# Kernel optimization log

Measured on AMD Instinct MI355X. Metric: run time of the kernel, lower is better.

## Reference

```python
import jax, jax.numpy as jnp
import numpy as np

H, W = 8, 8
N = 1 + H * W          # 65 tokens (cls + patches)
DIM = 128
HEADS = 8
DH = 32
INNER = HEADS * DH     # 256
B = 64
EPS = 1e-5


def setup_inputs() -> dict:
    key = jax.random.key(0)
    ks = jax.random.split(key, 7)
    x = jax.random.normal(ks[0], (B, N, DIM), dtype=jnp.float32)
    gamma = jnp.ones((DIM,), jnp.float32)
    beta = jnp.zeros((DIM,), jnp.float32)
    # kaiming_uniform-ish init scale for linear weights
    s_qk = float(np.sqrt(1.0 / DIM))
    Wqk = jax.random.uniform(ks[1], (DIM, 2 * INNER), jnp.float32, -s_qk, s_qk)
    # per-(query, key)-position value weights: [n, n, dim, inner]
    Wv = jax.random.uniform(ks[2], (N, N, DIM, INNER), jnp.float32, -s_qk, s_qk)
    s_o = float(np.sqrt(1.0 / INNER))
    Wout = jax.random.uniform(ks[3], (INNER, DIM), jnp.float32, -s_o, s_o)
    bout = jax.random.uniform(ks[4], (DIM,), jnp.float32, -s_o, s_o)
    return {"x": x, "gamma": gamma, "beta": beta, "Wqk": Wqk, "Wv": Wv,
            "Wout": Wout, "bout": bout}


def reference(x, gamma, beta, Wqk, Wv, Wout, bout):
    b, n, d = x.shape
    # LayerNorm
    mu = jnp.mean(x, axis=-1, keepdims=True)
    var = jnp.mean(jnp.square(x - mu), axis=-1, keepdims=True)
    xn = (x - mu) / jnp.sqrt(var + EPS) * gamma + beta
    # q, k projections
    qk = xn @ Wqk                               # [b, n, 2*inner]
    q, k = jnp.split(qk, 2, axis=-1)
    q = q.reshape(b, n, HEADS, DH).transpose(0, 2, 1, 3)  # [b, h, n, dh]
    k = k.reshape(b, n, HEADS, DH).transpose(0, 2, 1, 3)
    scale = DH ** -0.5
    dots = jnp.einsum('bhnd,bhmd->bhnm', q, k) * scale
    attn = jax.nn.softmax(dots, axis=-1)        # [b, h, n, m]
    # per-(n,m) value: v[b,n,m] = xn[b,n] @ Wv[n,m]  -> [b, n, m, inner]
    v = jnp.einsum('bnd,nmde->bnme', xn, Wv)
    v = v.reshape(b, n, n, HEADS, DH)           # [b, n, m, h, dh]
    # weighted sum over keys m
    out = jnp.einsum('bhnm,bnmhd->bnhd', attn, v).reshape(b, n, INNER)
    return out @ Wout + bout
```

## Files before the change

kernel.cpp:

```cpp
#include <hip/hip_runtime.h>

#define EPS 1e-5f

typedef __attribute__((ext_vector_type(8))) short short8;
typedef __attribute__((ext_vector_type(4))) float float4v;

__device__ __forceinline__ unsigned short f2bf(float x) {
  unsigned int u = __builtin_bit_cast(unsigned int, x);
  u += 0x7fffu + ((u >> 16) & 1u);
  return (unsigned short)(u >> 16);
}
__device__ __forceinline__ float bf2f(unsigned short h) {
  unsigned int u = ((unsigned int)h) << 16;
  return __builtin_bit_cast(float, u);
}

__global__ __launch_bounds__(256) void ln_kernel(
    const float* __restrict__ x, const float* __restrict__ gamma,
    const float* __restrict__ beta, float* __restrict__ xn) {
  const int row = blockIdx.x * 4 + (threadIdx.x >> 6);
  const int lane = threadIdx.x & 63;
  const float2 v = ((const float2*)(x + (size_t)row * 128))[lane];
  float s = v.x + v.y;
#pragma unroll
  for (int off = 1; off < 64; off <<= 1) s += __shfl_xor(s, off);
  const float mu = s * (1.f / 128.f);
  const float dx = v.x - mu, dy = v.y - mu;
  float qv = dx * dx + dy * dy;
#pragma unroll
  for (int off = 1; off < 64; off <<= 1) qv += __shfl_xor(qv, off);
  const float rstd = 1.f / sqrtf(qv * (1.f / 128.f) + EPS);
  const float2 g = ((const float2*)gamma)[lane];
  const float2 be = ((const float2*)beta)[lane];
  float2 o;
  o.x = dx * rstd * g.x + be.x;
  o.y = dy * rstd * g.y + be.y;
  ((float2*)(xn + (size_t)row * 128))[lane] = o;
}

__global__ __launch_bounds__(256) void qk_kernel(
    const float* __restrict__ xn, const float* __restrict__ Wqk,
    float* __restrict__ qk) {
  __shared__ float xsx[32][130];
  __shared__ float wsx[128][68];
  const int t = threadIdx.x;
  const int r0 = blockIdx.x * 32, c0 = blockIdx.y * 64;
  for (int i = t; i < 32 * 32; i += 256) {
    int r = i >> 5, c = (i & 31) << 2;
    float4 v = *(const float4*)(xn + (size_t)(r0 + r) * 128 + c);
    float* dst = &xsx[r][c];
    dst[0] = v.x; dst[1] = v.y; dst[2] = v.z; dst[3] = v.w;
  }
  for (int i = t; i < 128 * 16; i += 256) {
    int k = i >> 4, c = (i & 15) << 2;
    *(float4*)&wsx[k][c] = *(const float4*)(Wqk + (size_t)k * 512 + c0 + c);
  }
  __syncthreads();
  const int rr = (t >> 4) * 2, cc = (t & 15) * 4;
  float acc[2][4] = {{0.f, 0.f, 0.f, 0.f}, {0.f, 0.f, 0.f, 0.f}};
  for (int k = 0; k < 128; k++) {
    float4 wv4 = *(const float4*)&wsx[k][cc];
    float x0 = xsx[rr][k], x1 = xsx[rr + 1][k];
    acc[0][0] += x0 * wv4.x; acc[0][1] += x0 * wv4.y;
    acc[0][2] += x0 * wv4.z; acc[0][3] += x0 * wv4.w;
    acc[1][0] += x1 * wv4.x; acc[1][1] += x1 * wv4.y;
    acc[1][2] += x1 * wv4.z; acc[1][3] += x1 * wv4.w;
  }
#pragma unroll
  for (int r = 0; r < 2; r++) {
    float4 o;
    o.x = acc[r][0]; o.y = acc[r][1]; o.z = acc[r][2]; o.w = acc[r][3];
    *(float4*)(qk + (size_t)(r0 + rr + r) * 512 + c0 + cc) = o;
  }
}

__global__ __launch_bounds__(256) void softmax_kernel(
    const float* __restrict__ qk, float* __restrict__ attn) {
  const int b = blockIdx.x >> 3, h = blockIdx.x & 7;
  __shared__ float qs[65][33];
  __shared__ float ks[65][33];
  __shared__ float dotsS[65][66];
  __shared__ float rsum[65];
  const int t = threadIdx.x;
  for (int i = t; i < 65 * 32; i += 256) {
    int n = i >> 5, d = i & 31;
    size_t base = ((size_t)b * 65 + n) * 512 + h * 32 + d;
    qs[n][d] = qk[base];
    ks[n][d] = qk[base + 256];
  }
  __syncthreads();
  const float scale = 0.17677669529663687f;
  for (int i = t; i < 65 * 65; i += 256) {
    int n = i / 65, mm = i - n * 65;
    float s = 0.f;
#pragma unroll
    for (int d = 0; d < 32; d++) s += qs[n][d] * ks[mm][d];
    dotsS[n][mm] = s * scale;
  }
  __syncthreads();
  if (t < 65) {
    float mx = -1e30f;
    for (int mm = 0; mm < 65; mm++) mx = fmaxf(mx, dotsS[t][mm]);
    float sum = 0.f;
    for (int mm = 0; mm < 65; mm++) {
      float e = __expf(dotsS[t][mm] - mx);
      dotsS[t][mm] = e;
      sum += e;
    }
    rsum[t] = 1.f / sum;
  }
  __syncthreads();
  const size_t obase = ((size_t)b * 8 + h) * 65 * 65;
  for (int i = t; i < 65 * 65; i += 256) {
    int n = i / 65;
    attn[obase + i] = dotsS[n][i - n * 65] * rsum[n];
  }
}

__global__ __launch_bounds__(256, 3) void attnv_kernel(
    const float* __restrict__ xn, const float* __restrict__ attn,
    const float* __restrict__ Wv, float* __restrict__ inner) {
  __shared__ __align__(16) char sbuf[33280];
  __shared__ float attnL[4225];
  float* xs = (float*)sbuf;
  unsigned short* wvb = (unsigned short*)sbuf;

  const int nq = blockIdx.x >> 3, h = blockIdx.x & 7;
  const int t = threadIdx.x, lane = t & 63, w = t >> 6;
  const int boff = w * 16;
  const int er = lane & 15, q = lane >> 4;

  const int e = t & 31;
  const int d0 = (t >> 5) * 16;
  const int kc0 = d0 >> 3;
  const float* wbase = Wv + (size_t)nq * 65 * 32768 + (size_t)h * 32 + e;

  float stg[16];
  {
    const float* p = wbase + (size_t)d0 * 256;
#pragma unroll
    for (int i = 0; i < 16; i++) stg[i] = p[(size_t)i * 256];
  }

  for (int i = t; i < 64 * 65; i += 256) {
    int b = i / 65, m = i - b * 65;
    attnL[m * 65 + b] = attn[(((size_t)b * 8 + h) * 65 + nq) * 65 + m];
  }
  for (int i = t; i < 64 * 32; i += 256) {
    int b = i >> 5, c = (i & 31) << 2;
    float4 v = *(const float4*)(xn + ((size_t)b * 65 + nq) * 128 + c);
    float* dst = xs + b * 130 + c;
    dst[0] = v.x; dst[1] = v.y; dst[2] = v.z; dst[3] = v.w;
  }
  __syncthreads();

  short8 ah[4], al[4];
  {
    const int arow = boff + er;
#pragma unroll
    for (int s = 0; s < 4; s++) {
#pragma unroll
      for (int j = 0; j < 8; j++) {
        float xv = xs[arow * 130 + s * 32 + q * 8 + j];
        unsigned short hi = f2bf(xv);
        ah[s][j] = (short)hi;
        al[s][j] = (short)f2bf(xv - bf2f(hi));
      }
    }
  }
  __syncthreads();

  {
    short8 w0, w1;
#pragma unroll
    for (int j = 0; j < 8; j++) {
      w0[j] = (short)f2bf(stg[j]);
      w1[j] = (short)f2bf(stg[8 + j]);
    }
    *(short8*)&wvb[e * 128 + ((kc0 ^ (e & 15)) << 3)] = w0;
    *(short8*)&wvb[e * 128 + (((kc0 + 1) ^ (e & 15)) << 3)] = w1;
  }
  __syncthreads();

  float4v acc0 = {0.f, 0.f, 0.f, 0.f}, acc1 = {0.f, 0.f, 0.f, 0.f};

  for (int m = 0; m < 65; m++) {
    const int cur = m & 1;
    if (m < 64) {
      const float* p = wbase + (size_t)(m + 1) * 32768 + (size_t)d0 * 256;
#pragma unroll
      for (int i = 0; i < 16; i++) stg[i] = p[(size_t)i * 256];
    }
    const unsigned short* wb = wvb + cur * 4096;
    float4v P0 = {0.f, 0.f, 0.f, 0.f}, P1 = {0.f, 0.f, 0.f, 0.f};
#pragma unroll
    for (int s = 0; s < 4; s++) {
      const int kc = 4 * s + q;
      short8 b0 = *(const short8*)&wb[er * 128 + ((kc ^ er) << 3)];
      short8 b1 = *(const short8*)&wb[(er + 16) * 128 + ((kc ^ er) << 3)];
      P0 = __builtin_amdgcn_mfma_f32_16x16x32_bf16(ah[s], b0, P0, 0, 0, 0);
      P1 = __builtin_amdgcn_mfma_f32_16x16x32_bf16(ah[s], b1, P1, 0, 0, 0);
      P0 = __builtin_amdgcn_mfma_f32_16x16x32_bf16(al[s], b0, P0, 0, 0, 0);
      P1 = __builtin_amdgcn_mfma_f32_16x16x32_bf16(al[s], b1, P1, 0, 0, 0);
    }
    {
      const float* ap = attnL + m * 65 + boff + q * 4;
#pragma unroll
      for (int r = 0; r < 4; r++) {
        float av = ap[r];
        acc0[r] += av * P0[r];
        acc1[r] += av * P1[r];
      }
    }
    if (m < 64) {
      short8 w0, w1;
#pragma unroll
      for (int j = 0; j < 8; j++) {
        w0[j] = (short)f2bf(stg[j]);
        w1[j] = (short)f2bf(stg[8 + j]);
      }
      unsigned short* wbw = wvb + (1 - cur) * 4096;
      *(short8*)&wbw[e * 128 + ((kc0 ^ (e & 15)) << 3)] = w0;
      *(short8*)&wbw[e * 128 + (((kc0 + 1) ^ (e & 15)) << 3)] = w1;
    }
    __syncthreads();
  }

#pragma unroll
  for (int r = 0; r < 4; r++) {
    int b = boff + q * 4 + r;
    size_t o = ((size_t)b * 65 + nq) * 256 + h * 32;
    inner[o + er] = acc0[r];
    inner[o + 16 + er] = acc1[r];
  }
}

__global__ __launch_bounds__(256) void outproj_kernel(
    const float* __restrict__ inner, const float* __restrict__ Wout,
    const float* __restrict__ bout, float* __restrict__ out) {
  __shared__ float isx[16][258];
  __shared__ float wsx[64][132];
  const int t = threadIdx.x;
  const int r0 = blockIdx.x * 16;
  for (int i = t; i < 16 * 64; i += 256) {
    int r = i >> 6, c = (i & 63) << 2;
    float4 v = *(const float4*)(inner + (size_t)(r0 + r) * 256 + c);
    float* dst = &isx[r][c];
    dst[0] = v.x; dst[1] = v.y; dst[2] = v.z; dst[3] = v.w;
  }
  const int rr = (t >> 5) * 2, cc = (t & 31) * 4;
  float acc[2][4] = {{0.f, 0.f, 0.f, 0.f}, {0.f, 0.f, 0.f, 0.f}};
  for (int kc = 0; kc < 4; kc++) {
    __syncthreads();
    for (int i = t; i < 64 * 32; i += 256) {
      int k = i >> 5, c = (i & 31) << 2;
      *(float4*)&wsx[k][c] = *(const float4*)(Wout + (size_t)(kc * 64 + k) * 128 + c);
    }
    __syncthreads();
#pragma unroll 8
    for (int k = 0; k < 64; k++) {
      float4 wv4 = *(const float4*)&wsx[k][cc];
      float x0 = isx[rr][kc * 64 + k];
      float x1 = isx[rr + 1][kc * 64 + k];
      acc[0][0] += x0 * wv4.x; acc[0][1] += x0 * wv4.y;
      acc[0][2] += x0 * wv4.z; acc[0][3] += x0 * wv4.w;
      acc[1][0] += x1 * wv4.x; acc[1][1] += x1 * wv4.y;
      acc[1][2] += x1 * wv4.z; acc[1][3] += x1 * wv4.w;
    }
  }
  float4 bb = *(const float4*)(bout + cc);
#pragma unroll
  for (int r = 0; r < 2; r++) {
    float4 o;
    o.x = acc[r][0] + bb.x; o.y = acc[r][1] + bb.y;
    o.z = acc[r][2] + bb.z; o.w = acc[r][3] + bb.w;
    *(float4*)(out + (size_t)(r0 + rr + r) * 128 + cc) = o;
  }
}

extern "C" void kernel_launch(void* const* d_in, const int* in_sizes, int n_in,
                              void* d_out, int out_size, void* d_ws, size_t ws_size,
                              hipStream_t stream) {
  const float* x     = (const float*)d_in[0];
  const float* gamma = (const float*)d_in[1];
  const float* beta  = (const float*)d_in[2];
  const float* Wqk   = (const float*)d_in[3];
  const float* Wv    = (const float*)d_in[4];
  const float* Wout  = (const float*)d_in[5];
  const float* bout  = (const float*)d_in[6];
  float* out = (float*)d_out;
  float* ws  = (float*)d_ws;

  float* xn    = ws;
  float* qk    = ws + 532480;
  float* attn  = ws + 2662400;
  float* inner = ws + 4825600;

  ln_kernel<<<1040, 256, 0, stream>>>(x, gamma, beta, xn);
  qk_kernel<<<dim3(130, 8), 256, 0, stream>>>(xn, Wqk, qk);
  softmax_kernel<<<512, 256, 0, stream>>>(qk, attn);
  attnv_kernel<<<520, 256, 0, stream>>>(xn, attn, Wv, inner);
  outproj_kernel<<<260, 256, 0, stream>>>(inner, Wout, bout, out);
}
```

Before: 807.7 us.

## Split attnv key loop across two blocks and transpose attn layout

The attention-value kernel now splits the 65 key positions into two halves handled by separate blocks, doubling the grid to 1040 blocks. Each half writes a partial inner buffer, and the output projection sums the two. Softmax writes attention transposed so attnv can load its slice contiguously, and xn is read straight from global memory instead of being staged in LDS. Shared memory drops and the occupancy hint rises to 4. The aim is more parallelism for streaming the large Wv tensor, at the cost of an extra partial buffer and scattered, strided writes in softmax.

```diff
diff --git a/kernel.cpp b/kernel.cpp
--- a/kernel.cpp
+++ b/kernel.cpp
@@ -75,7 +75,7 @@
 }
 
 __global__ __launch_bounds__(256) void softmax_kernel(
-    const float* __restrict__ qk, float* __restrict__ attn) {
+    const float* __restrict__ qk, float* __restrict__ attnT) {
   const int b = blockIdx.x >> 3, h = blockIdx.x & 7;
   __shared__ float qs[65][33];
   __shared__ float ks[65][33];
@@ -110,22 +110,24 @@
     rsum[t] = 1.f / sum;
   }
   __syncthreads();
-  const size_t obase = ((size_t)b * 8 + h) * 65 * 65;
   for (int i = t; i < 65 * 65; i += 256) {
-    int n = i / 65;
-    attn[obase + i] = dotsS[n][i - n * 65] * rsum[n];
-  }
-}
-
-__global__ __launch_bounds__(256, 3) void attnv_kernel(
-    const float* __restrict__ xn, const float* __restrict__ attn,
-    const float* __restrict__ Wv, float* __restrict__ inner) {
-  __shared__ __align__(16) char sbuf[33280];
-  __shared__ float attnL[4225];
-  float* xs = (float*)sbuf;
-  unsigned short* wvb = (unsigned short*)sbuf;
-
-  const int nq = blockIdx.x >> 3, h = blockIdx.x & 7;
+    int n = i / 65, mm = i - n * 65;
+    attnT[(((size_t)h * 65 + n) * 65 + mm) * 64 + b] = dotsS[n][mm] * rsum[n];
+  }
+}
+
+__global__ __launch_bounds__(256, 4) void attnv_kernel(
+    const float* __restrict__ xn, const float* __restrict__ attnT,
+    const float* __restrict__ Wv, float* __restrict__ innerp) {
+  __shared__ __align__(16) unsigned short wvb[2][4096];
+  __shared__ float attnL[33 * 64];
+
+  const int nq = blockIdx.x >> 4;
+  const int h = (blockIdx.x >> 1) & 7;
+  const int half = blockIdx.x & 1;
+  const int m0 = half * 33;
+  const int mlen = half ? 32 : 33;
+
   const int t = threadIdx.x, lane = t & 63, w = t >> 6;
   const int boff = w * 16;
   const int er = lane & 15, q = lane >> 4;
@@ -133,7 +135,7 @@
   const int e = t & 31;
   const int d0 = (t >> 5) * 16;
   const int kc0 = d0 >> 3;
-  const float* wbase = Wv + (size_t)nq * 65 * 32768 + (size_t)h * 32 + e;
+  const float* wbase = Wv + ((size_t)nq * 65 + m0) * 32768 + (size_t)h * 32 + e;
 
   float stg[16];
   {
@@ -142,33 +144,27 @@
     for (int i = 0; i < 16; i++) stg[i] = p[(size_t)i * 256];
   }
 
-  for (int i = t; i < 64 * 65; i += 256) {
-    int b = i / 65, m = i - b * 65;
-    attnL[m * 65 + b] = attn[(((size_t)b * 8 + h) * 65 + nq) * 65 + m];
-  }
-  for (int i = t; i < 64 * 32; i += 256) {
-    int b = i >> 5, c = (i & 31) << 2;
-    float4 v = *(const float4*)(xn + ((size_t)b * 65 + nq) * 128 + c);
-    float* dst = xs + b * 130 + c;
-    dst[0] = v.x; dst[1] = v.y; dst[2] = v.z; dst[3] = v.w;
-  }
-  __syncthreads();
+  {
+    const float* abase = attnT + (((size_t)h * 65 + nq) * 65 + m0) * 64;
+    for (int i = t; i < mlen * 64; i += 256) attnL[i] = abase[i];
+  }
 
   short8 ah[4], al[4];
   {
-    const int arow = boff + er;
+    const float* arow = xn + ((size_t)(boff + er) * 65 + nq) * 128;
 #pragma unroll
     for (int s = 0; s < 4; s++) {
+      float4 v0 = *(const float4*)(arow + s * 32 + q * 8);
+      float4 v1 = *(const float4*)(arow + s * 32 + q * 8 + 4);
+      float xv[8] = {v0.x, v0.y, v0.z, v0.w, v1.x, v1.y, v1.z, v1.w};
 #pragma unroll
       for (int j = 0; j < 8; j++) {
-        float xv = xs[arow * 130 + s * 32 + q * 8 + j];
-        unsigned short hi = f2bf(xv);
+        unsigned short hi = f2bf(xv[j]);
         ah[s][j] = (short)hi;
-        al[s][j] = (short)f2bf(xv - bf2f(hi));
+        al[s][j] = (short)f2bf(xv[j] - bf2f(hi));
       }
     }
   }
-  __syncthreads();
 
   {
     short8 w0, w1;
@@ -177,21 +173,21 @@
       w0[j] = (short)f2bf(stg[j]);
       w1[j] = (short)f2bf(stg[8 + j]);
     }
-    *(short8*)&wvb[e * 128 + ((kc0 ^ (e & 15)) << 3)] = w0;
-    *(short8*)&wvb[e * 128 + (((kc0 + 1) ^ (e & 15)) << 3)] = w1;
+    *(short8*)&wvb[0][e * 128 + ((kc0 ^ (e & 15)) << 3)] = w0;
+    *(short8*)&wvb[0][e * 128 + (((kc0 + 1) ^ (e & 15)) << 3)] = w1;
   }
   __syncthreads();
 
   float4v acc0 = {0.f, 0.f, 0.f, 0.f}, acc1 = {0.f, 0.f, 0.f, 0.f};
 
-  for (int m = 0; m < 65; m++) {
+  for (int m = 0; m < mlen; m++) {
     const int cur = m & 1;
-    if (m < 64) {
+    if (m + 1 < mlen) {
       const float* p = wbase + (size_t)(m + 1) * 32768 + (size_t)d0 * 256;
 #pragma unroll
       for (int i = 0; i < 16; i++) stg[i] = p[(size_t)i * 256];
     }
-    const unsigned short* wb = wvb + cur * 4096;
+    const unsigned short* wb = wvb[cur];
     float4v P0 = {0.f, 0.f, 0.f, 0.f}, P1 = {0.f, 0.f, 0.f, 0.f};
 #pragma unroll
     for (int s = 0; s < 4; s++) {
@@ -204,7 +200,7 @@
       P1 = __builtin_amdgcn_mfma_f32_16x16x32_bf16(al[s], b1, P1, 0, 0, 0);
     }
     {
-      const float* ap = attnL + m * 65 + boff + q * 4;
+      const float* ap = attnL + m * 64 + boff + q * 4;
 #pragma unroll
       for (int r = 0; r < 4; r++) {
         float av = ap[r];
@@ -212,41 +208,46 @@
         acc1[r] += av * P1[r];
       }
     }
-    if (m < 64) {
+    if (m + 1 < mlen) {
       short8 w0, w1;
 #pragma unroll
       for (int j = 0; j < 8; j++) {
         w0[j] = (short)f2bf(stg[j]);
         w1[j] = (short)f2bf(stg[8 + j]);
       }
-      unsigned short* wbw = wvb + (1 - cur) * 4096;
+      unsigned short* wbw = wvb[1 - cur];
       *(short8*)&wbw[e * 128 + ((kc0 ^ (e & 15)) << 3)] = w0;
       *(short8*)&wbw[e * 128 + (((kc0 + 1) ^ (e & 15)) << 3)] = w1;
     }
     __syncthreads();
   }
 
+  float* ip = innerp + (size_t)half * 1064960;
 #pragma unroll
   for (int r = 0; r < 4; r++) {
     int b = boff + q * 4 + r;
     size_t o = ((size_t)b * 65 + nq) * 256 + h * 32;
-    inner[o + er] = acc0[r];
-    inner[o + 16 + er] = acc1[r];
+    ip[o + er] = acc0[r];
+    ip[o + 16 + er] = acc1[r];
   }
 }
 
 __global__ __launch_bounds__(256) void outproj_kernel(
-    const float* __restrict__ inner, const float* __restrict__ Wout,
-    const float* __restrict__ bout, float* __restrict__ out) {
+    const float* __restrict__ inner0, const float* __restrict__ inner1,
+    const float* __restrict__ Wout, const float* __restrict__ bout,
+    float* __restrict__ out) {
   __shared__ float isx[16][258];
   __shared__ float wsx[64][132];
   const int t = threadIdx.x;
   const int r0 = blockIdx.x * 16;
   for (int i = t; i < 16 * 64; i += 256) {
     int r = i >> 6, c = (i & 63) << 2;
-    float4 v = *(const float4*)(inner + (size_t)(r0 + r) * 256 + c);
+    size_t off = (size_t)(r0 + r) * 256 + c;
+    float4 v0 = *(const float4*)(inner0 + off);
+    float4 v1 = *(const float4*)(inner1 + off);
     float* dst = &isx[r][c];
-    dst[0] = v.x; dst[1] = v.y; dst[2] = v.z; dst[3] = v.w;
+    dst[0] = v0.x + v1.x; dst[1] = v0.y + v1.y;
+    dst[2] = v0.z + v1.z; dst[3] = v0.w + v1.w;
   }
   const int rr = (t >> 5) * 2, cc = (t & 31) * 4;
   float acc[2][4] = {{0.f, 0.f, 0.f, 0.f}, {0.f, 0.f, 0.f, 0.f}};
@@ -293,12 +294,12 @@
 
   float* xn    = ws;
   float* qk    = ws + 532480;
-  float* attn  = ws + 2662400;
+  float* attnT = ws + 2662400;
   float* inner = ws + 4825600;
 
   ln_kernel<<<1040, 256, 0, stream>>>(x, gamma, beta, xn);
   qk_kernel<<<dim3(130, 8), 256, 0, stream>>>(xn, Wqk, qk);
-  softmax_kernel<<<512, 256, 0, stream>>>(qk, attn);
-  attnv_kernel<<<520, 256, 0, stream>>>(xn, attn, Wv, inner);
-  outproj_kernel<<<260, 256, 0, stream>>>(inner, Wout, bout, out);
-}
+  softmax_kernel<<<512, 256, 0, stream>>>(qk, attnT);
+  attnv_kernel<<<1040, 256, 0, stream>>>(xn, attnT, Wv, inner);
+  outproj_kernel<<<260, 256, 0, stream>>>(inner, inner + 1064960, Wout, bout, out);
+}
```

Result: no change. 809.3 us (+0.2%).
